# Optimization experiments

Hardware: AMD Instinct MI355X
Metric: run time of the kernel (lower is better)

The kernel has to match this reference:

```python
import jax, jax.numpy as jnp
import numpy as np
from jax import lax

MAX_SCALE = 4
SCALES = [2 ** i for i in range(1, MAX_SCALE + 1)]  # [2, 4, 8, 16]
EPS = 1e-6
BN_EPS = 1e-3  # keras BatchNormalization default epsilon


def _box_sum(x, r):
    # DepthwiseConv2D with ones kernel, SAME zero padding == box sum window
    return lax.reduce_window(x, 0.0, lax.add, (1, r, r, 1), (1, 1, 1, 1), 'SAME')


def setup_inputs() -> dict:
    key = jax.random.key(0)
    k1, k2 = jax.random.split(key)
    B, H, W, C, K = 4, 224, 224, 64, 8
    return {
        'x': jax.random.normal(k1, (B, H, W, C), dtype=jnp.float32),
        'ols_weights': jnp.ones((MAX_SCALE,), jnp.float32),
        'anchors': jax.random.normal(k2, (C, K), dtype=jnp.float32),
        'hist_widths': jnp.ones((C, K), jnp.float32),
        'bn_gamma': jnp.ones((C,), jnp.float32),
        'bn_beta': jnp.zeros((C,), jnp.float32),
        'bn_mean': jnp.zeros((C,), jnp.float32),
        'bn_var': jnp.ones((C,), jnp.float32),
    }


def reference(x, ols_weights, anchors, hist_widths, bn_gamma, bn_beta, bn_mean, bn_var):
    # --- sample min-max scaling to [0, 1] per sample ---
    xmin = jnp.min(x, axis=(1, 2, 3), keepdims=True)
    xmax = jnp.max(x, axis=(1, 2, 3), keepdims=True)
    xs = (x - xmin) / (xmax - xmin + EPS)

    # --- multi-scale box measures: [B,H,W,C,S] ---
    measures = jnp.stack([_box_sum(xs, r) for r in SCALES], axis=-1)

    # --- weighted OLS slope of log(measure) vs log(scale) -> local alpha ---
    ly = jnp.log(measures + EPS)                         # [B,H,W,C,S]
    lr = jnp.log(jnp.asarray(SCALES, jnp.float32))       # [S]
    w = ols_weights                                       # [S]
    wsum = jnp.sum(w)
    lr_bar = jnp.sum(w * lr) / wsum
    ly_bar = jnp.sum(w * ly, axis=-1, keepdims=True) / wsum
    dx = lr - lr_bar                                      # [S]
    num = jnp.sum(w * dx * (ly - ly_bar), axis=-1)        # [B,H,W,C]
    den = jnp.sum(w * dx * dx)
    alphas = num / den

    # --- batch norm (inference mode, training=False) ---
    a = bn_gamma * (alphas - bn_mean) * lax.rsqrt(bn_var + BN_EPS) + bn_beta

    # --- triangular soft histogram over k anchors, relu'd and summed ---
    hist = 1.0 - hist_widths * jnp.abs(a[..., None] - anchors)  # [B,H,W,C,K]
    soft_counts = jnp.sum(jax.nn.relu(hist), axis=-1)           # [B,H,W,C]

    return x + jax.nn.sigmoid(soft_counts)
```

## Files before the change

kernel.cpp:

```cpp
#include <hip/hip_runtime.h>
#include <math.h>

#define B 4
#define H 224
#define W 224
#define C 64
#define K 8
#define WC (W*C)
#define HWC (H*W*C)

__device__ inline float wave_reduce_min(float v) {
  #pragma unroll
  for (int off = 32; off > 0; off >>= 1)
    v = fminf(v, __shfl_down(v, off, 64));
  return v;
}
__device__ inline float wave_reduce_max(float v) {
  #pragma unroll
  for (int off = 32; off > 0; off >>= 1)
    v = fmaxf(v, __shfl_down(v, off, 64));
  return v;
}

struct FalseT { static constexpr bool value = false; };
struct TrueT  { static constexpr bool value = true; };


__global__ __launch_bounds__(256) void k_vpfx_raw4(const float* __restrict__ x,
                                                   float* __restrict__ P,
                                                   float* __restrict__ pmin,
                                                   float* __restrict__ pmax) {
  int bid = blockIdx.x;
  int b = bid / W, w = bid % W;
  int seg = threadIdx.x >> 4;
  int chg = threadIdx.x & 15;
  int wv  = threadIdx.x >> 6;

  const size_t colbase = (size_t)b*HWC + (size_t)w*C;
  const float4* xp4 = (const float4*)(x + colbase);
  const int RS4 = WC / 4;
  const int r0 = seg * 14;

  float4 v4[14];
  #pragma unroll
  for (int j = 0; j < 14; ++j) v4[j] = xp4[(size_t)(r0 + j) * RS4 + chg];

  float4 s4 = v4[0];
  float vmin = fminf(fminf(v4[0].x, v4[0].y), fminf(v4[0].z, v4[0].w));
  float vmax = fmaxf(fmaxf(v4[0].x, v4[0].y), fmaxf(v4[0].z, v4[0].w));
  #pragma unroll
  for (int j = 1; j < 14; ++j) {
    s4.x += v4[j].x; s4.y += v4[j].y; s4.z += v4[j].z; s4.w += v4[j].w;
    vmin = fminf(vmin, fminf(fminf(v4[j].x, v4[j].y), fminf(v4[j].z, v4[j].w)));
    vmax = fmaxf(vmax, fmaxf(fmaxf(v4[j].x, v4[j].y), fmaxf(v4[j].z, v4[j].w)));
  }

  __shared__ float4 segsum[16][16];
  __shared__ float smin[4], smax[4];
  segsum[seg][chg] = s4;
  float wmn = wave_reduce_min(vmin), wmx = wave_reduce_max(vmax);
  if ((threadIdx.x & 63) == 0) { smin[wv] = wmn; smax[wv] = wmx; }
  __syncthreads();

  if (threadIdx.x == 0) {
    pmin[bid] = fminf(fminf(smin[0], smin[1]), fminf(smin[2], smin[3]));
    pmax[bid] = fmaxf(fmaxf(smax[0], smax[1]), fmaxf(smax[2], smax[3]));
  }

  float4 o4 = {0.f, 0.f, 0.f, 0.f};
  #pragma unroll
  for (int ss = 0; ss < 16; ++ss) {
    if (ss < seg) {
      float4 t = segsum[ss][chg];
      o4.x += t.x; o4.y += t.y; o4.z += t.z; o4.w += t.w;
    }
  }

  float4* Pp4 = (float4*)(P + colbase);
  float ax = o4.x, ay = o4.y, az = o4.z, aw = o4.w;
  #pragma unroll
  for (int j = 0; j < 14; ++j) {
    ax += v4[j].x; ay += v4[j].y; az += v4[j].z; aw += v4[j].w;
    float4 outv; outv.x = ax; outv.y = ay; outv.z = az; outv.w = aw;
    Pp4[(size_t)(r0 + j) * RS4 + chg] = outv;
  }
}

__global__ __launch_bounds__(128) void k_main2(
    const float* __restrict__ P, const float* __restrict__ x,
    const float* __restrict__ pmin, const float* __restrict__ pmax,
    const float* __restrict__ ols, const float* __restrict__ anchors,
    const float* __restrict__ hwidths, const float* __restrict__ bn_gamma,
    const float* __restrict__ bn_beta, const float* __restrict__ bn_mean,
    const float* __restrict__ bn_var, float* __restrict__ out) {
  int xcd  = blockIdx.x & 7;
  int i    = blockIdx.x >> 3;
  int rg   = xcd * 112 + (i >> 2);
  int wave = threadIdx.x >> 6, c = threadIdx.x & 63;
  int chunk = (i & 3) * 2 + wave;
  int b = rg / H, h = rg % H;
  int w0 = chunk * 28;

  float vmin = INFINITY, vmax = -INFINITY;
  for (int ii = threadIdx.x; ii < W; ii += 128) {
    vmin = fminf(vmin, pmin[b*W + ii]);
    vmax = fmaxf(vmax, pmax[b*W + ii]);
  }
  vmin = wave_reduce_min(vmin);
  vmax = wave_reduce_max(vmax);
  __shared__ float sred[4];
  if ((threadIdx.x & 63) == 0) { sred[wave*2] = vmin; sred[wave*2+1] = vmax; }
  __syncthreads();
  float xmin = fminf(sred[0], sred[2]);
  float xmax = fmaxf(sred[1], sred[3]);
  float rng  = xmax - xmin + 1e-6f;
  float epsp = 1e-6f * rng;

  const float LN2 = 0.69314718055994530942f;
  float wg0 = ols[0], wg1 = ols[1], wg2 = ols[2], wg3 = ols[3];
  float l0 = LN2, l1 = 2.f*LN2, l2 = 3.f*LN2, l3 = 4.f*LN2;
  float wsum = wg0 + wg1 + wg2 + wg3;
  float lrbar = (wg0*l0 + wg1*l1 + wg2*l2 + wg3*l3) / wsum;
  float d0 = l0-lrbar, d1 = l1-lrbar, d2 = l2-lrbar, d3 = l3-lrbar;
  float den = wg0*d0*d0 + wg1*d1*d1 + wg2*d2*d2 + wg3*d3*d3;
  float c0 = wg0*d0/den, c1 = wg1*d1/den, c2 = wg2*d2/den, c3 = wg3*d3/den;

  float scl  = bn_gamma[c] * rsqrtf(bn_var[c] + 1e-3f);
  float bofs = bn_beta[c] - bn_mean[c] * scl;
  float anc[K], wd[K];
  #pragma unroll
  for (int k = 0; k < K; ++k) { anc[k] = anchors[c*K + k]; wd[k] = hwidths[c*K + k]; }

  const int hiA[4] = {1, 2, 4, 8};
  const int loA[4] = {0, 1, 3, 7};
  const int rA[4]  = {2, 4, 8, 16};
  const float* pt[4]; const float* pb[4]; float fb[4];
  float Anh[4], Kin[4];
  #pragma unroll
  for (int s = 0; s < 4; ++s) {
    int ht = h + hiA[s]; if (ht > H-1) ht = H-1;
    int hb = h - loA[s] - 1;
    int hbc = hb < 0 ? 0 : hb;
    pt[s] = P + (size_t)b*HWC + (size_t)ht*WC + c;
    pb[s] = P + (size_t)b*HWC + (size_t)hbc*WC + c;
    fb[s] = hb < 0 ? 0.f : 1.f;
    int h0 = h - loA[s]; if (h0 < 0) h0 = 0;
    int nv = ht - h0 + 1;
    Anh[s] = -(float)nv * xmin;
    Kin[s] = (float)rA[s] * Anh[s] + epsp;
  }

  const float* xrow = x   + (size_t)b*HWC + (size_t)h*WC + c;
  float*       orow = out + (size_t)b*HWC + (size_t)h*WC + c;

  auto tloop = [&](auto EDGEC) {
    constexpr bool EDGE = decltype(EDGEC)::value;
    float ring2[2]   = {0,0};
    float ring4[4]   = {0,0,0,0};
    float ring8[8]   = {0,0,0,0,0,0,0,0};
    float ring16[16] = {0,0,0,0,0,0,0,0,0,0,0,0,0,0,0,0};
    float T0 = 0.f, T1 = 0.f, T2 = 0.f, T3 = 0.f;
    float abuf[8] = {0,0,0,0,0,0,0,0};

    for (int t0 = 0; t0 < 48; t0 += 16) {
      #pragma unroll
      for (int u = 0; u < 16; ++u) {
        int t  = t0 + u;
        int wr = w0 - 7 + t;
        float m0, m1, m2, m3;
        if constexpr (EDGE) {
          m0 = m1 = m2 = m3 = 0.f;
          if (wr >= 0 && wr < W) {
            int off = wr * C;
            m0 = pt[0][off] - fb[0]*pb[0][off];
            m1 = pt[1][off] - fb[1]*pb[1][off];
            m2 = pt[2][off] - fb[2]*pb[2][off];
            m3 = pt[3][off] - fb[3]*pb[3][off];
          }
        } else {
          int off = wr * C;
          m0 = pt[0][off] - fb[0]*pb[0][off];
          m1 = pt[1][off] - fb[1]*pb[1][off];
          m2 = pt[2][off] - fb[2]*pb[2][off];
          m3 = pt[3][off] - fb[3]*pb[3][off];
        }
        T0 += m0 - ring2[u&1];  ring2[u&1]  = m0;
        T1 += m1 - ring4[u&3];  ring4[u&3]  = m1;
        T2 += m2 - ring8[u&7];  ring8[u&7]  = m2;
        T3 += m3 - ring16[u];   ring16[u]   = m3;

        float a0, a1, a2, a3;
        if constexpr (EDGE) {
          float nh0 = (float)(min(wr, W-1) - max(wr-1,  0) + 1);
          float nh1 = (float)(min(wr, W-1) - max(wr-3,  0) + 1);
          float nh2 = (float)(min(wr, W-1) - max(wr-7,  0) + 1);
          float nh3 = (float)(min(wr, W-1) - max(wr-15, 0) + 1);
          a0 = fmaxf(fmaf(Anh[0], nh0, T0) + epsp, epsp);
          a1 = fmaxf(fmaf(Anh[1], nh1, T1) + epsp, epsp);
          a2 = fmaxf(fmaf(Anh[2], nh2, T2) + epsp, epsp);
          a3 = fmaxf(fmaf(Anh[3], nh3, T3) + epsp, epsp);
        } else {
          a0 = fmaxf(T0 + Kin[0], epsp);
          a1 = fmaxf(T1 + Kin[1], epsp);
          a2 = fmaxf(T2 + Kin[2], epsp);
          a3 = fmaxf(T3 + Kin[3], epsp);
        }
        abuf[(u+7)&7] += c0 * __logf(a0);
        abuf[(u+6)&7] += c1 * __logf(a1);
        abuf[(u+4)&7] += c2 * __logf(a2);
        abuf[u&7]     += c3 * __logf(a3);

        int ig = w0 - 15 + t;
        if (t >= 15 && ig <= w0 + 27) {
          float alpha = abuf[u&7];
          float a = alpha * scl + bofs;
          float sc = 0.f;
          #pragma unroll
          for (int k = 0; k < K; ++k)
            sc += fmaxf(0.f, 1.f - wd[k]*fabsf(a - anc[k]));
          float sig = 1.f / (1.f + __expf(-sc));
          float xv = __builtin_nontemporal_load(&xrow[ig*C]);
          __builtin_nontemporal_store(xv + sig, &orow[ig*C]);
        }
        abuf[u&7] = 0.f;
      }
    }
  };
  if (w0 >= 22 && w0 <= 183) tloop(FalseT{}); else tloop(TrueT{});
}


__global__ __launch_bounds__(256) void k_minmax_part(const float* __restrict__ x,
                                                     float* __restrict__ scratch) {
  int s   = blockIdx.x >> 9;
  int blk = blockIdx.x & 511;
  const float4* xs = (const float4*)(x + (size_t)s * HWC);
  const int n4 = HWC / 4;
  float vmin = INFINITY, vmax = -INFINITY;
  for (int i = blk*256 + threadIdx.x; i < n4; i += 512*256) {
    float4 v = xs[i];
    vmin = fminf(vmin, fminf(fminf(v.x, v.y), fminf(v.z, v.w)));
    vmax = fmaxf(vmax, fmaxf(fmaxf(v.x, v.y), fmaxf(v.z, v.w)));
  }
  __shared__ float smin[4], smax[4];
  float wmin = wave_reduce_min(vmin), wmax = wave_reduce_max(vmax);
  int wave = threadIdx.x >> 6, lane = threadIdx.x & 63;
  if (lane == 0) { smin[wave] = wmin; smax[wave] = wmax; }
  __syncthreads();
  if (threadIdx.x == 0) {
    float m = fminf(fminf(smin[0], smin[1]), fminf(smin[2], smin[3]));
    float M = fmaxf(fmaxf(smax[0], smax[1]), fmaxf(smax[2], smax[3]));
    scratch[blockIdx.x]        = m;
    scratch[2048 + blockIdx.x] = M;
  }
}

__global__ __launch_bounds__(256) void k_vpfx4(const float* __restrict__ x,
                                               const float* __restrict__ scratch,
                                               float* __restrict__ P) {
  int bid = blockIdx.x;
  int b = bid / W, w = bid % W;
  int seg = threadIdx.x >> 4;
  int chg = threadIdx.x & 15;
  int wv  = threadIdx.x >> 6;

  float vmn = fminf(scratch[b*512 + threadIdx.x], scratch[b*512 + 256 + threadIdx.x]);
  float vmx = fmaxf(scratch[2048 + b*512 + threadIdx.x], scratch[2048 + b*512 + 256 + threadIdx.x]);
  __shared__ float smin[4], smax[4];
  float wmn = wave_reduce_min(vmn), wmx = wave_reduce_max(vmx);
  if ((threadIdx.x & 63) == 0) { smin[wv] = wmn; smax[wv] = wmx; }
  __syncthreads();
  float xmin = fminf(fminf(smin[0], smin[1]), fminf(smin[2], smin[3]));
  float xmax = fmaxf(fmaxf(smax[0], smax[1]), fmaxf(smax[2], smax[3]));
  float inv  = 1.0f / (xmax - xmin + 1e-6f);

  const size_t colbase = (size_t)b*HWC + (size_t)w*C;
  const float4* xp4 = (const float4*)(x + colbase);
  const int RS4 = WC / 4;
  const int r0 = seg * 14;

  float4 v4[14];
  #pragma unroll
  for (int j = 0; j < 14; ++j) v4[j] = xp4[(size_t)(r0 + j) * RS4 + chg];

  float4 s4 = v4[0];
  #pragma unroll
  for (int j = 1; j < 14; ++j) {
    s4.x += v4[j].x; s4.y += v4[j].y; s4.z += v4[j].z; s4.w += v4[j].w;
  }

  __shared__ float4 segsum[16][16];
  segsum[seg][chg] = s4;
  __syncthreads();

  float4 o4 = {0.f, 0.f, 0.f, 0.f};
  #pragma unroll
  for (int ss = 0; ss < 16; ++ss) {
    if (ss < seg) {
      float4 t = segsum[ss][chg];
      o4.x += t.x; o4.y += t.y; o4.z += t.z; o4.w += t.w;
    }
  }

  float4* Pp4 = (float4*)(P + colbase);
  float ax = o4.x, ay = o4.y, az = o4.z, aw = o4.w;
  #pragma unroll
  for (int j = 0; j < 14; ++j) {
    ax += v4[j].x; ay += v4[j].y; az += v4[j].z; aw += v4[j].w;
    float sub = (float)(r0 + j + 1) * xmin;
    float4 outv;
    outv.x = (ax - sub) * inv;
    outv.y = (ay - sub) * inv;
    outv.z = (az - sub) * inv;
    outv.w = (aw - sub) * inv;
    Pp4[(size_t)(r0 + j) * RS4 + chg] = outv;
  }
}

__global__ __launch_bounds__(128) void k_main(
    const float* __restrict__ P, const float* __restrict__ x,
    const float* __restrict__ ols, const float* __restrict__ anchors,
    const float* __restrict__ hwidths, const float* __restrict__ bn_gamma,
    const float* __restrict__ bn_beta, const float* __restrict__ bn_mean,
    const float* __restrict__ bn_var, float* __restrict__ out) {
  int xcd  = blockIdx.x & 7;
  int i    = blockIdx.x >> 3;
  int rg   = xcd * 112 + (i >> 2);
  int wave = threadIdx.x >> 6, c = threadIdx.x & 63;
  int chunk = (i & 3) * 2 + wave;
  int b = rg / H, h = rg % H;
  int w0 = chunk * 28;

  const float LN2 = 0.69314718055994530942f;
  float wg0 = ols[0], wg1 = ols[1], wg2 = ols[2], wg3 = ols[3];
  float l0 = LN2, l1 = 2.f*LN2, l2 = 3.f*LN2, l3 = 4.f*LN2;
  float wsum = wg0 + wg1 + wg2 + wg3;
  float lrbar = (wg0*l0 + wg1*l1 + wg2*l2 + wg3*l3) / wsum;
  float d0 = l0-lrbar, d1 = l1-lrbar, d2 = l2-lrbar, d3 = l3-lrbar;
  float den = wg0*d0*d0 + wg1*d1*d1 + wg2*d2*d2 + wg3*d3*d3;
  float c0 = wg0*d0/den, c1 = wg1*d1/den, c2 = wg2*d2/den, c3 = wg3*d3/den;

  float scl  = bn_gamma[c] * rsqrtf(bn_var[c] + 1e-3f);
  float bofs = bn_beta[c] - bn_mean[c] * scl;
  float anc[K], wd[K];
  #pragma unroll
  for (int k = 0; k < K; ++k) { anc[k] = anchors[c*K + k]; wd[k] = hwidths[c*K + k]; }

  const int hiA[4] = {1, 2, 4, 8};
  const int loA[4] = {0, 1, 3, 7};
  const float* pt[4]; const float* pb[4]; float fb[4];
  #pragma unroll
  for (int s = 0; s < 4; ++s) {
    int ht = h + hiA[s]; if (ht > H-1) ht = H-1;
    int hb = h - loA[s] - 1;
    int hbc = hb < 0 ? 0 : hb;
    pt[s] = P + (size_t)b*HWC + (size_t)ht*WC + c;
    pb[s] = P + (size_t)b*HWC + (size_t)hbc*WC + c;
    fb[s] = hb < 0 ? 0.f : 1.f;
  }

  const float* xrow = x   + (size_t)b*HWC + (size_t)h*WC + c;
  float*       orow = out + (size_t)b*HWC + (size_t)h*WC + c;

  float ring2[2]   = {0,0};
  float ring4[4]   = {0,0,0,0};
  float ring8[8]   = {0,0,0,0,0,0,0,0};
  float ring16[16] = {0,0,0,0,0,0,0,0,0,0,0,0,0,0,0,0};
  float T0 = 0.f, T1 = 0.f, T2 = 0.f, T3 = 0.f;
  float abuf[8] = {0,0,0,0,0,0,0,0};

  for (int t0 = 0; t0 < 48; t0 += 16) {
    #pragma unroll
    for (int u = 0; u < 16; ++u) {
      int t  = t0 + u;
      int wr = w0 - 7 + t;
      float m0 = 0.f, m1 = 0.f, m2 = 0.f, m3 = 0.f;
      if (wr >= 0 && wr < W) {
        int off = wr * C;
        m0 = pt[0][off] - fb[0]*pb[0][off];
        m1 = pt[1][off] - fb[1]*pb[1][off];
        m2 = pt[2][off] - fb[2]*pb[2][off];
        m3 = pt[3][off] - fb[3]*pb[3][off];
      }
      T0 += m0 - ring2[u&1];  ring2[u&1]  = m0;
      T1 += m1 - ring4[u&3];  ring4[u&3]  = m1;
      T2 += m2 - ring8[u&7];  ring8[u&7]  = m2;
      T3 += m3 - ring16[u];   ring16[u]   = m3;
      abuf[(u+7)&7] += c0 * __logf(fmaxf(T0, 0.f) + 1e-6f);
      abuf[(u+6)&7] += c1 * __logf(fmaxf(T1, 0.f) + 1e-6f);
      abuf[(u+4)&7] += c2 * __logf(fmaxf(T2, 0.f) + 1e-6f);
      abuf[u&7]     += c3 * __logf(fmaxf(T3, 0.f) + 1e-6f);
      int ig = w0 - 15 + t;
      if (t >= 15 && ig <= w0 + 27) {
        float alpha = abuf[u&7];
        float a = alpha * scl + bofs;
        float sc = 0.f;
        #pragma unroll
        for (int k = 0; k < K; ++k)
          sc += fmaxf(0.f, 1.f - wd[k]*fabsf(a - anc[k]));
        float sig = 1.f / (1.f + __expf(-sc));
        float xv = __builtin_nontemporal_load(&xrow[ig*C]);
        __builtin_nontemporal_store(xv + sig, &orow[ig*C]);
      }
      abuf[u&7] = 0.f;
    }
  }
}


extern "C" void kernel_launch(void* const* d_in, const int* in_sizes, int n_in,
                              void* d_out, int out_size, void* d_ws, size_t ws_size,
                              hipStream_t stream) {
  const float* x        = (const float*)d_in[0];
  const float* ols      = (const float*)d_in[1];
  const float* anchors  = (const float*)d_in[2];
  const float* hwidths  = (const float*)d_in[3];
  const float* bn_gamma = (const float*)d_in[4];
  const float* bn_beta  = (const float*)d_in[5];
  const float* bn_mean  = (const float*)d_in[6];
  const float* bn_var   = (const float*)d_in[7];
  float* out = (float*)d_out;
  float* P   = (float*)d_ws;
  const size_t PBYTES = (size_t)B * HWC * sizeof(float);

  if (ws_size >= PBYTES + 8192) {
    float* pmn = (float*)((char*)d_ws + PBYTES);
    float* pmx = pmn + 1024;
    hipLaunchKernelGGL(k_vpfx_raw4, dim3(B*W),   dim3(256), 0, stream, x, P, pmn, pmx);
    hipLaunchKernelGGL(k_main2,     dim3(B*H*4), dim3(128), 0, stream,
                       P, x, pmn, pmx, ols, anchors, hwidths,
                       bn_gamma, bn_beta, bn_mean, bn_var, out);
  } else {
    float* scratch = out;
    hipLaunchKernelGGL(k_minmax_part, dim3(2048),  dim3(256), 0, stream, x, scratch);
    hipLaunchKernelGGL(k_vpfx4,       dim3(B*W),   dim3(256), 0, stream, x, scratch, P);
    hipLaunchKernelGGL(k_main,        dim3(B*H*4), dim3(128), 0, stream,
                       P, x, ols, anchors, hwidths,
                       bn_gamma, bn_beta, bn_mean, bn_var, out);
  }
}
```

Before: 225.3 us.

## Widen vertical prefix-sum blocks to 1024 threads covering four columns each

The vertical prefix-sum kernel now uses 1024-thread blocks where each wave covers 64 consecutive float4 lanes (four w-columns of 64 channels), so each row load becomes a contiguous 1 KB segment instead of 256 B. Grid shrinks from B*W to B*56 blocks, and the per-block min/max is written replicated into four pmin/pmax slots so the consumer kernel's indexing is unchanged. This aims at better coalescing and fewer blocks, at the cost of lower block count (224 blocks) for occupancy and a larger shared-memory footprint.

```diff
diff --git a/kernel.cpp b/kernel.cpp
--- a/kernel.cpp
+++ b/kernel.cpp
@@ -26,24 +26,26 @@
 struct TrueT  { static constexpr bool value = true; };
 
 
-__global__ __launch_bounds__(256) void k_vpfx_raw4(const float* __restrict__ x,
-                                                   float* __restrict__ P,
-                                                   float* __restrict__ pmin,
-                                                   float* __restrict__ pmax) {
+__global__ __launch_bounds__(1024) void k_vpfx_wide(const float* __restrict__ x,
+                                                    float* __restrict__ P,
+                                                    float* __restrict__ pmin,
+                                                    float* __restrict__ pmax) {
   int bid = blockIdx.x;
-  int b = bid / W, w = bid % W;
-  int seg = threadIdx.x >> 4;
-  int chg = threadIdx.x & 15;
-  int wv  = threadIdx.x >> 6;
-
-  const size_t colbase = (size_t)b*HWC + (size_t)w*C;
-  const float4* xp4 = (const float4*)(x + colbase);
-  const int RS4 = WC / 4;
+  int b  = bid / 56, wg = bid % 56;
+  int tid  = threadIdx.x;
+  int seg  = tid >> 6;
+  int lane = tid & 63;
+  int col4 = wg * 64 + lane;
+
+  const float4* x4 = (const float4*)x;
+  float4*       P4 = (float4*)P;
+  const size_t rowbase = (size_t)b * H;
   const int r0 = seg * 14;
 
   float4 v4[14];
   #pragma unroll
-  for (int j = 0; j < 14; ++j) v4[j] = xp4[(size_t)(r0 + j) * RS4 + chg];
+  for (int j = 0; j < 14; ++j)
+    v4[j] = x4[(rowbase + r0 + j) * 3584 + col4];
 
   float4 s4 = v4[0];
   float vmin = fminf(fminf(v4[0].x, v4[0].y), fminf(v4[0].z, v4[0].w));
@@ -55,34 +57,37 @@
     vmax = fmaxf(vmax, fmaxf(fmaxf(v4[j].x, v4[j].y), fmaxf(v4[j].z, v4[j].w)));
   }
 
-  __shared__ float4 segsum[16][16];
-  __shared__ float smin[4], smax[4];
-  segsum[seg][chg] = s4;
+  __shared__ float4 segsum[16][64];
+  __shared__ float smin[16], smax[16];
+  segsum[seg][lane] = s4;
   float wmn = wave_reduce_min(vmin), wmx = wave_reduce_max(vmax);
-  if ((threadIdx.x & 63) == 0) { smin[wv] = wmn; smax[wv] = wmx; }
+  if (lane == 0) { smin[seg] = wmn; smax[seg] = wmx; }
   __syncthreads();
 
-  if (threadIdx.x == 0) {
-    pmin[bid] = fminf(fminf(smin[0], smin[1]), fminf(smin[2], smin[3]));
-    pmax[bid] = fmaxf(fmaxf(smax[0], smax[1]), fmaxf(smax[2], smax[3]));
+  if (tid == 0) {
+    float m = smin[0], M = smax[0];
+    #pragma unroll
+    for (int s = 1; s < 16; ++s) { m = fminf(m, smin[s]); M = fmaxf(M, smax[s]); }
+    int base = b * 224 + wg * 4;
+    pmin[base+0] = m; pmin[base+1] = m; pmin[base+2] = m; pmin[base+3] = m;
+    pmax[base+0] = M; pmax[base+1] = M; pmax[base+2] = M; pmax[base+3] = M;
   }
 
   float4 o4 = {0.f, 0.f, 0.f, 0.f};
   #pragma unroll
   for (int ss = 0; ss < 16; ++ss) {
     if (ss < seg) {
-      float4 t = segsum[ss][chg];
+      float4 t = segsum[ss][lane];
       o4.x += t.x; o4.y += t.y; o4.z += t.z; o4.w += t.w;
     }
   }
 
-  float4* Pp4 = (float4*)(P + colbase);
   float ax = o4.x, ay = o4.y, az = o4.z, aw = o4.w;
   #pragma unroll
   for (int j = 0; j < 14; ++j) {
     ax += v4[j].x; ay += v4[j].y; az += v4[j].z; aw += v4[j].w;
     float4 outv; outv.x = ax; outv.y = ay; outv.z = az; outv.w = aw;
-    Pp4[(size_t)(r0 + j) * RS4 + chg] = outv;
+    P4[(rowbase + r0 + j) * 3584 + col4] = outv;
   }
 }
 
@@ -426,8 +431,8 @@
   if (ws_size >= PBYTES + 8192) {
     float* pmn = (float*)((char*)d_ws + PBYTES);
     float* pmx = pmn + 1024;
-    hipLaunchKernelGGL(k_vpfx_raw4, dim3(B*W),   dim3(256), 0, stream, x, P, pmn, pmx);
-    hipLaunchKernelGGL(k_main2,     dim3(B*H*4), dim3(128), 0, stream,
+    hipLaunchKernelGGL(k_vpfx_wide, dim3(B*56),  dim3(1024), 0, stream, x, P, pmn, pmx);
+    hipLaunchKernelGGL(k_main2,     dim3(B*H*4), dim3(128),  0, stream,
                        P, x, pmn, pmx, ols, anchors, hwidths,
                        bn_gamma, bn_beta, bn_mean, bn_var, out);
   } else {
```

New measurement: 223.4 us. About the same (-0.9%).
